# Performance work log

Hardware: AMD Instinct MI355X
Metric: run time of the kernel (lower is better)

Reference implementation:

```python
import jax, jax.numpy as jnp
import numpy as np


def setup_inputs() -> dict:
    key = jax.random.key(0)
    ks = jax.random.split(key, 8)
    Bsz, L, D, N, R = 2, 2048, 2048, 16, 128
    x = jax.random.normal(ks[0], (Bsz, L, D), jnp.float32)
    delta = jax.random.normal(ks[1], (Bsz, L, R), jnp.float32)
    B_in = jax.random.normal(ks[2], (Bsz, L, N), jnp.float32)
    C_in = jax.random.normal(ks[3], (Bsz, L, N), jnp.float32)
    # dt_proj params (scaled small so softplus(dt) stays in a sane range)
    W_dt = jax.random.normal(ks[4], (D, R), jnp.float32) * 0.02
    b_dt = jax.random.normal(ks[5], (D,), jnp.float32) * 0.02
    # A_log = log(uniform(0,1)) as in the torch init -> A = -exp(A_log) in (-1, 0)
    A_log = jnp.log(jax.random.uniform(ks[6], (D, N), jnp.float32, 1e-4, 1.0))
    D_param = jnp.ones((D,), jnp.float32)
    return {"x": x, "delta": delta, "B_in": B_in, "C_in": C_in,
            "W_dt": W_dt, "b_dt": b_dt, "A_log": A_log, "D_param": D_param}


def reference(x, delta, B_in, C_in, W_dt, b_dt, A_log, D_param):
    # dt = softplus(dt_proj(delta))  -> (B, L, D)
    dt = jax.nn.softplus(jnp.einsum('blr,dr->bld', delta, W_dt) + b_dt)
    A = -jnp.exp(A_log)                                  # (D, N)
    decay = jnp.exp(jnp.einsum('bld,dn->bldn', dt, A))   # exp(dt*A): (B, L, D, N)
    u = jnp.einsum('bld,bln->bldn', dt * x, B_in)        # dt*B*x input term
    # move length to leading axis for scan
    aT = jnp.moveaxis(decay, 1, 0)   # (L, B, D, N)
    uT = jnp.moveaxis(u, 1, 0)       # (L, B, D, N)
    cT = jnp.moveaxis(C_in, 1, 0)    # (L, B, N)

    h0 = jnp.zeros((x.shape[0], x.shape[2], A.shape[1]), x.dtype)  # (B, D, N)

    def step(h, inp):
        a, uu, c = inp
        h = a * h + uu                              # selective state update
        y = jnp.einsum('bdn,bn->bd', h, c)          # readout
        return h, y

    _, ys = jax.lax.scan(step, h0, (aT, uT, cT))    # ys: (L, B, D)
    return jnp.moveaxis(ys, 0, 1) + x * D_param
```

## Files before the change

### kernel.cpp

```cpp
#include <hip/hip_runtime.h>
#include <hip/hip_bf16.h>
#include <math.h>

namespace {

constexpr int BSZ = 2, LEN = 2048, DIM = 2048, NST = 16, RNK = 128;
constexpr int NC = 64, CHUNK = LEN / NC;
constexpr int KS = 3 * RNK;
constexpr float LOG2E = 1.4426950408889634f;
constexpr float LN2 = 0.6931471805599453f;

using bf16x8 = __attribute__((ext_vector_type(8))) short;
using f32x4  = __attribute__((ext_vector_type(4))) float;

__device__ __forceinline__ float fast_exp2(float x) {
#if __has_builtin(__builtin_amdgcn_exp2f)
  return __builtin_amdgcn_exp2f(x);
#else
  return exp2f(x);
#endif
}

__device__ __forceinline__ unsigned short bf16_rne(float x) {
  __hip_bfloat16 h = __float2bfloat16(x);
  return *(unsigned short*)&h;
}
__device__ __forceinline__ float bf16_tof(unsigned short u) {
  __hip_bfloat16 h = *(__hip_bfloat16*)&u;
  return __bfloat162float(h);
}

__global__ __launch_bounds__(256)
void split_bf16(const float* __restrict__ delta, const float* __restrict__ W,
                unsigned short* __restrict__ Ad, unsigned short* __restrict__ Bd) {
  int t = blockIdx.x * 256 + threadIdx.x;
  const int NA = BSZ * LEN * RNK;
  if (t < NA) {
    int row = t >> 7, k = t & (RNK - 1);
    float x = delta[t];
    unsigned short hi = bf16_rne(x);
    unsigned short lo = bf16_rne(x - bf16_tof(hi));
    unsigned short* p = Ad + (size_t)row * KS;
    p[k] = hi; p[RNK + k] = lo; p[2 * RNK + k] = hi;
  } else {
    t -= NA;
    int row = t >> 7, k = t & (RNK - 1);
    float x = W[t];
    unsigned short hi = bf16_rne(x);
    unsigned short lo = bf16_rne(x - bf16_tof(hi));
    unsigned short* p = Bd + (size_t)row * KS;
    p[k] = hi; p[RNK + k] = hi; p[2 * RNK + k] = lo;
  }
}

__global__ __launch_bounds__(256)
void dt_mfma(const unsigned short* __restrict__ Ad, const unsigned short* __restrict__ Bd,
             const float* __restrict__ bias, float* __restrict__ dtout) {
  const int lane = threadIdx.x & 63, wid = threadIdx.x >> 6;
  const int wm = wid >> 1, wn = wid & 1;
  const int bm = blockIdx.x & 31, bn = blockIdx.x >> 5;
  const int r = lane & 15, kg = lane >> 4;

  const unsigned short* arow = Ad + (size_t)(bm * 128 + wm * 64 + r) * KS + kg * 8;
  const unsigned short* brow = Bd + (size_t)(bn * 128 + wn * 64 + r) * KS + kg * 8;

  f32x4 acc[4][4] = {};
#pragma unroll
  for (int ks = 0; ks < KS / 32; ++ks) {
    bf16x8 af[4], bf[4];
#pragma unroll
    for (int m = 0; m < 4; ++m)
      af[m] = *(const bf16x8*)(arow + (size_t)m * 16 * KS + ks * 32);
#pragma unroll
    for (int n = 0; n < 4; ++n)
      bf[n] = *(const bf16x8*)(brow + (size_t)n * 16 * KS + ks * 32);
#pragma unroll
    for (int m = 0; m < 4; ++m)
#pragma unroll
      for (int n = 0; n < 4; ++n)
        acc[m][n] = __builtin_amdgcn_mfma_f32_16x16x32_bf16(af[m], bf[n], acc[m][n], 0, 0, 0);
  }

#pragma unroll
  for (int n = 0; n < 4; ++n) {
    const int col = bn * 128 + wn * 64 + n * 16 + r;
    const float bs = bias[col];
#pragma unroll
    for (int m = 0; m < 4; ++m) {
      const int row0 = bm * 128 + wm * 64 + m * 16 + kg * 4;
#pragma unroll
      for (int j = 0; j < 4; ++j) {
        float z = acc[m][n][j] + bs;
        float sp = fmaxf(z, 0.f) + LN2 * __log2f(1.0f + fast_exp2(-fabsf(z) * LOG2E));
        dtout[(size_t)(row0 + j) * DIM + col] = sp;
      }
    }
  }
}

__global__ __launch_bounds__(256)
void scan_pass1(const float* __restrict__ dtw, const float* __restrict__ x,
                const float* __restrict__ Bin, const float* __restrict__ Alog,
                float* __restrict__ Pout, float* __restrict__ Sout) {
  __shared__ float4 Bl[CHUNK * NST / 4];
  const int tid = threadIdx.x;
  const int bz = blockIdx.x;
  const int dt8 = bz & 7;
  const int c = (bz >> 3) & (NC - 1);
  const int b = bz >> 9;
  const int d = dt8 * 256 + tid;
  const int l0 = c * CHUNK;

  if (tid < CHUNK * NST / 4)
    Bl[tid] = ((const float4*)(Bin + ((size_t)b * LEN + l0) * NST))[tid];

  float A2[NST];
  {
    const float4* ap = (const float4*)(Alog + (size_t)d * NST);
#pragma unroll
    for (int q = 0; q < 4; ++q) {
      float4 v = ap[q];
      A2[q * 4 + 0] = -expf(v.x) * LOG2E;
      A2[q * 4 + 1] = -expf(v.y) * LOG2E;
      A2[q * 4 + 2] = -expf(v.z) * LOG2E;
      A2[q * 4 + 3] = -expf(v.w) * LOG2E;
    }
  }
  __syncthreads();

  float h[NST];
#pragma unroll
  for (int n = 0; n < NST; ++n) h[n] = 0.f;
  float sdt = 0.f;
  const float* dtp = dtw + ((size_t)b * LEN + l0) * DIM + d;
  const float* xp  = x   + ((size_t)b * LEN + l0) * DIM + d;

  float dtc = dtp[0], xc = xp[0];
#pragma unroll 4
  for (int i = 0; i < CHUNK; ++i) {
    float dtn = 0.f, xn = 0.f;
    if (i + 1 < CHUNK) { dtn = dtp[(size_t)(i + 1) * DIM]; xn = xp[(size_t)(i + 1) * DIM]; }
    float dtx = dtc * xc;
    sdt += dtc;
#pragma unroll
    for (int q = 0; q < 4; ++q) {
      float4 Bv = Bl[i * 4 + q];
      float e0 = fast_exp2(dtc * A2[q * 4 + 0]);
      float e1 = fast_exp2(dtc * A2[q * 4 + 1]);
      float e2 = fast_exp2(dtc * A2[q * 4 + 2]);
      float e3 = fast_exp2(dtc * A2[q * 4 + 3]);
      h[q * 4 + 0] = fmaf(e0, h[q * 4 + 0], dtx * Bv.x);
      h[q * 4 + 1] = fmaf(e1, h[q * 4 + 1], dtx * Bv.y);
      h[q * 4 + 2] = fmaf(e2, h[q * 4 + 2], dtx * Bv.z);
      h[q * 4 + 3] = fmaf(e3, h[q * 4 + 3], dtx * Bv.w);
    }
    dtc = dtn; xc = xn;
  }

  const size_t obase = ((size_t)(b * NC + c) * DIM + d) * NST;
#pragma unroll
  for (int q = 0; q < 4; ++q) {
    float4 pv;
    pv.x = fast_exp2(sdt * A2[q * 4 + 0]);
    pv.y = fast_exp2(sdt * A2[q * 4 + 1]);
    pv.z = fast_exp2(sdt * A2[q * 4 + 2]);
    pv.w = fast_exp2(sdt * A2[q * 4 + 3]);
    *(float4*)&Pout[obase + q * 4] = pv;
    float4 sv = {h[q * 4 + 0], h[q * 4 + 1], h[q * 4 + 2], h[q * 4 + 3]};
    *(float4*)&Sout[obase + q * 4] = sv;
  }
}

__global__ __launch_bounds__(256)
void chunk_combine(float* __restrict__ P, const float* __restrict__ S) {
  const int t = blockIdx.x * 256 + threadIdx.x;
  const int n = t & (NST - 1);
  const int d = (t >> 4) & (DIM - 1);
  const int b = t >> 15;
  float cur = 0.f;
#pragma unroll 8
  for (int c = 0; c < NC; ++c) {
    const size_t idx = ((size_t)(b * NC + c) * DIM + d) * NST + n;
    float p = P[idx];
    float s = S[idx];
    P[idx] = cur;
    cur = fmaf(p, cur, s);
  }
}

__global__ __launch_bounds__(256)
void scan_pass2(const float* __restrict__ dtw, const float* __restrict__ x,
                const float* __restrict__ Bin, const float* __restrict__ Cin,
                const float* __restrict__ Alog, const float* __restrict__ Dpar,
                const float* __restrict__ Hin, float* __restrict__ out) {
  __shared__ float4 Bl[CHUNK * NST / 4];
  __shared__ float4 Cl[CHUNK * NST / 4];
  const int tid = threadIdx.x;
  const int bz = blockIdx.x;
  const int dt8 = bz & 7;
  const int c = (bz >> 3) & (NC - 1);
  const int b = bz >> 9;
  const int d = dt8 * 256 + tid;
  const int l0 = c * CHUNK;

  if (tid < CHUNK * NST / 4)
    Bl[tid] = ((const float4*)(Bin + ((size_t)b * LEN + l0) * NST))[tid];
  else if (tid < CHUNK * NST / 2)
    Cl[tid - CHUNK * NST / 4] = ((const float4*)(Cin + ((size_t)b * LEN + l0) * NST))[tid - CHUNK * NST / 4];

  float A2[NST];
  {
    const float4* ap = (const float4*)(Alog + (size_t)d * NST);
#pragma unroll
    for (int q = 0; q < 4; ++q) {
      float4 v = ap[q];
      A2[q * 4 + 0] = -expf(v.x) * LOG2E;
      A2[q * 4 + 1] = -expf(v.y) * LOG2E;
      A2[q * 4 + 2] = -expf(v.z) * LOG2E;
      A2[q * 4 + 3] = -expf(v.w) * LOG2E;
    }
  }

  const size_t obase = ((size_t)(b * NC + c) * DIM + d) * NST;
  float h[NST];
#pragma unroll
  for (int q = 0; q < 4; ++q) {
    float4 hv = *(const float4*)&Hin[obase + q * 4];
    h[q * 4 + 0] = hv.x; h[q * 4 + 1] = hv.y; h[q * 4 + 2] = hv.z; h[q * 4 + 3] = hv.w;
  }
  const float dpar = Dpar[d];
  __syncthreads();

  const float* dtp = dtw + ((size_t)b * LEN + l0) * DIM + d;
  const float* xp  = x   + ((size_t)b * LEN + l0) * DIM + d;
  float* op        = out + ((size_t)b * LEN + l0) * DIM + d;

  float dtc = dtp[0], xc = xp[0];
#pragma unroll 4
  for (int i = 0; i < CHUNK; ++i) {
    float dtn = 0.f, xn = 0.f;
    if (i + 1 < CHUNK) { dtn = dtp[(size_t)(i + 1) * DIM]; xn = xp[(size_t)(i + 1) * DIM]; }
    float dtx = dtc * xc;
    float y0 = 0.f, y1 = 0.f, y2 = 0.f, y3 = 0.f;
#pragma unroll
    for (int q = 0; q < 4; ++q) {
      float4 Bv = Bl[i * 4 + q];
      float4 Cv = Cl[i * 4 + q];
      float e0 = fast_exp2(dtc * A2[q * 4 + 0]);
      float e1 = fast_exp2(dtc * A2[q * 4 + 1]);
      float e2 = fast_exp2(dtc * A2[q * 4 + 2]);
      float e3 = fast_exp2(dtc * A2[q * 4 + 3]);
      float hh0 = fmaf(e0, h[q * 4 + 0], dtx * Bv.x);
      float hh1 = fmaf(e1, h[q * 4 + 1], dtx * Bv.y);
      float hh2 = fmaf(e2, h[q * 4 + 2], dtx * Bv.z);
      float hh3 = fmaf(e3, h[q * 4 + 3], dtx * Bv.w);
      h[q * 4 + 0] = hh0; h[q * 4 + 1] = hh1; h[q * 4 + 2] = hh2; h[q * 4 + 3] = hh3;
      float yq = hh0 * Cv.x;
      yq = fmaf(hh1, Cv.y, yq);
      yq = fmaf(hh2, Cv.z, yq);
      yq = fmaf(hh3, Cv.w, yq);
      if (q == 0) y0 = yq; else if (q == 1) y1 = yq; else if (q == 2) y2 = yq; else y3 = yq;
    }
    op[(size_t)i * DIM] = fmaf(xc, dpar, (y0 + y1) + (y2 + y3));
    dtc = dtn; xc = xn;
  }
}

}

extern "C" void kernel_launch(void* const* d_in, const int* in_sizes, int n_in,
                              void* d_out, int out_size, void* d_ws, size_t ws_size,
                              hipStream_t stream) {
  const float* x     = (const float*)d_in[0];
  const float* delta = (const float*)d_in[1];
  const float* Bin   = (const float*)d_in[2];
  const float* Cin   = (const float*)d_in[3];
  const float* Wdt   = (const float*)d_in[4];
  const float* bdt   = (const float*)d_in[5];
  const float* Alog  = (const float*)d_in[6];
  const float* Dpar  = (const float*)d_in[7];
  float* out = (float*)d_out;

  char* ws = (char*)d_ws;
  size_t off = 0;
  float* dtw = (float*)(ws + off); off += (size_t)BSZ * LEN * DIM * 4;
  float* P   = (float*)(ws + off); off += (size_t)BSZ * NC * DIM * NST * 4;
  float* S   = (float*)(ws + off); off += (size_t)BSZ * NC * DIM * NST * 4;
  unsigned short* Ad = (unsigned short*)(ws + off); off += (size_t)BSZ * LEN * KS * 2;
  unsigned short* Bd = (unsigned short*)(ws + off); off += (size_t)DIM * KS * 2;

  split_bf16<<<(BSZ * LEN * RNK + DIM * RNK) / 256, 256, 0, stream>>>(delta, Wdt, Ad, Bd);
  dt_mfma<<<(BSZ * LEN / 128) * (DIM / 128), 256, 0, stream>>>(Ad, Bd, bdt, dtw);
  scan_pass1<<<BSZ * NC * (DIM / 256), 256, 0, stream>>>(dtw, x, Bin, Alog, P, S);
  chunk_combine<<<BSZ * DIM * NST / 256, 256, 0, stream>>>(P, S);
  scan_pass2<<<BSZ * NC * (DIM / 256), 256, 0, stream>>>(dtw, x, Bin, Cin, Alog, Dpar, P, out);
}
```

Measured before the change: 185.0 us.

## Fuse dt projection GEMM into both scan passes and drop P buffer

Removes the standalone dt GEMM kernel and its 32 MB dt workspace. Each scan block now recomputes its 32x256 dt tile with MFMA into shared memory, and both passes read dt from LDS instead of global memory. Pass 1 also writes only the per-chunk sum of dt instead of the full decay product P, and chunk_combine rebuilds the decay from Alog. The cost is running the GEMM twice (once per pass) and using 32 KB of extra LDS per block, which may lower occupancy.

```diff
diff --git a/kernel.cpp b/kernel.cpp
--- a/kernel.cpp
+++ b/kernel.cpp
@@ -53,66 +53,66 @@
   }
 }
 
-__global__ __launch_bounds__(256)
-void dt_mfma(const unsigned short* __restrict__ Ad, const unsigned short* __restrict__ Bd,
-             const float* __restrict__ bias, float* __restrict__ dtout) {
-  const int lane = threadIdx.x & 63, wid = threadIdx.x >> 6;
-  const int wm = wid >> 1, wn = wid & 1;
-  const int bm = blockIdx.x & 31, bn = blockIdx.x >> 5;
+__device__ __forceinline__ void compute_dt_tile(
+    const unsigned short* __restrict__ Ad, const unsigned short* __restrict__ Bd,
+    const float* __restrict__ bias, int b, int l0, int dgrp,
+    float (*dt_tile)[256]) {
+  const int lane = threadIdx.x & 63, w = threadIdx.x >> 6;
   const int r = lane & 15, kg = lane >> 4;
-
-  const unsigned short* arow = Ad + (size_t)(bm * 128 + wm * 64 + r) * KS + kg * 8;
-  const unsigned short* brow = Bd + (size_t)(bn * 128 + wn * 64 + r) * KS + kg * 8;
-
-  f32x4 acc[4][4] = {};
+  const unsigned short* arow = Ad + (size_t)(b * LEN + l0 + r) * KS + kg * 8;
+  const unsigned short* brow = Bd + (size_t)(dgrp * 256 + w * 64 + r) * KS + kg * 8;
+
+  f32x4 acc[2][4] = {};
 #pragma unroll
   for (int ks = 0; ks < KS / 32; ++ks) {
-    bf16x8 af[4], bf[4];
-#pragma unroll
-    for (int m = 0; m < 4; ++m)
-      af[m] = *(const bf16x8*)(arow + (size_t)m * 16 * KS + ks * 32);
+    bf16x8 af[2], bfr[4];
+    af[0] = *(const bf16x8*)(arow + ks * 32);
+    af[1] = *(const bf16x8*)(arow + (size_t)16 * KS + ks * 32);
 #pragma unroll
     for (int n = 0; n < 4; ++n)
-      bf[n] = *(const bf16x8*)(brow + (size_t)n * 16 * KS + ks * 32);
-#pragma unroll
-    for (int m = 0; m < 4; ++m)
+      bfr[n] = *(const bf16x8*)(brow + (size_t)n * 16 * KS + ks * 32);
+#pragma unroll
+    for (int m = 0; m < 2; ++m)
 #pragma unroll
       for (int n = 0; n < 4; ++n)
-        acc[m][n] = __builtin_amdgcn_mfma_f32_16x16x32_bf16(af[m], bf[n], acc[m][n], 0, 0, 0);
-  }
-
+        acc[m][n] = __builtin_amdgcn_mfma_f32_16x16x32_bf16(af[m], bfr[n], acc[m][n], 0, 0, 0);
+  }
 #pragma unroll
   for (int n = 0; n < 4; ++n) {
-    const int col = bn * 128 + wn * 64 + n * 16 + r;
-    const float bs = bias[col];
-#pragma unroll
-    for (int m = 0; m < 4; ++m) {
-      const int row0 = bm * 128 + wm * 64 + m * 16 + kg * 4;
+    const int dl = w * 64 + n * 16 + r;
+    const float bs = bias[dgrp * 256 + dl];
+#pragma unroll
+    for (int m = 0; m < 2; ++m) {
+      const int row0 = m * 16 + kg * 4;
 #pragma unroll
       for (int j = 0; j < 4; ++j) {
         float z = acc[m][n][j] + bs;
         float sp = fmaxf(z, 0.f) + LN2 * __log2f(1.0f + fast_exp2(-fabsf(z) * LOG2E));
-        dtout[(size_t)(row0 + j) * DIM + col] = sp;
+        dt_tile[row0 + j][dl] = sp;
       }
     }
   }
 }
 
 __global__ __launch_bounds__(256)
-void scan_pass1(const float* __restrict__ dtw, const float* __restrict__ x,
-                const float* __restrict__ Bin, const float* __restrict__ Alog,
-                float* __restrict__ Pout, float* __restrict__ Sout) {
+void scan1_fused(const unsigned short* __restrict__ Ad, const unsigned short* __restrict__ Bd,
+                 const float* __restrict__ bias, const float* __restrict__ x,
+                 const float* __restrict__ Bin, const float* __restrict__ Alog,
+                 float* __restrict__ Sout, float* __restrict__ sdtout) {
+  __shared__ float dt_tile[CHUNK][256];
   __shared__ float4 Bl[CHUNK * NST / 4];
   const int tid = threadIdx.x;
   const int bz = blockIdx.x;
-  const int dt8 = bz & 7;
+  const int dgrp = bz & 7;
   const int c = (bz >> 3) & (NC - 1);
   const int b = bz >> 9;
-  const int d = dt8 * 256 + tid;
+  const int d = dgrp * 256 + tid;
   const int l0 = c * CHUNK;
 
   if (tid < CHUNK * NST / 4)
     Bl[tid] = ((const float4*)(Bin + ((size_t)b * LEN + l0) * NST))[tid];
+
+  compute_dt_tile(Ad, Bd, bias, b, l0, dgrp, dt_tile);
 
   float A2[NST];
   {
@@ -132,81 +132,82 @@
 #pragma unroll
   for (int n = 0; n < NST; ++n) h[n] = 0.f;
   float sdt = 0.f;
-  const float* dtp = dtw + ((size_t)b * LEN + l0) * DIM + d;
-  const float* xp  = x   + ((size_t)b * LEN + l0) * DIM + d;
-
-  float dtc = dtp[0], xc = xp[0];
+  const float* xp = x + ((size_t)b * LEN + l0) * DIM + d;
+
+  float xc = xp[0];
 #pragma unroll 4
   for (int i = 0; i < CHUNK; ++i) {
-    float dtn = 0.f, xn = 0.f;
-    if (i + 1 < CHUNK) { dtn = dtp[(size_t)(i + 1) * DIM]; xn = xp[(size_t)(i + 1) * DIM]; }
-    float dtx = dtc * xc;
-    sdt += dtc;
+    float xn = 0.f;
+    if (i + 1 < CHUNK) xn = xp[(size_t)(i + 1) * DIM];
+    float dt = dt_tile[i][tid];
+    float dtx = dt * xc;
+    sdt += dt;
 #pragma unroll
     for (int q = 0; q < 4; ++q) {
       float4 Bv = Bl[i * 4 + q];
-      float e0 = fast_exp2(dtc * A2[q * 4 + 0]);
-      float e1 = fast_exp2(dtc * A2[q * 4 + 1]);
-      float e2 = fast_exp2(dtc * A2[q * 4 + 2]);
-      float e3 = fast_exp2(dtc * A2[q * 4 + 3]);
+      float e0 = fast_exp2(dt * A2[q * 4 + 0]);
+      float e1 = fast_exp2(dt * A2[q * 4 + 1]);
+      float e2 = fast_exp2(dt * A2[q * 4 + 2]);
+      float e3 = fast_exp2(dt * A2[q * 4 + 3]);
       h[q * 4 + 0] = fmaf(e0, h[q * 4 + 0], dtx * Bv.x);
       h[q * 4 + 1] = fmaf(e1, h[q * 4 + 1], dtx * Bv.y);
       h[q * 4 + 2] = fmaf(e2, h[q * 4 + 2], dtx * Bv.z);
       h[q * 4 + 3] = fmaf(e3, h[q * 4 + 3], dtx * Bv.w);
     }
-    dtc = dtn; xc = xn;
+    xc = xn;
   }
 
   const size_t obase = ((size_t)(b * NC + c) * DIM + d) * NST;
 #pragma unroll
   for (int q = 0; q < 4; ++q) {
-    float4 pv;
-    pv.x = fast_exp2(sdt * A2[q * 4 + 0]);
-    pv.y = fast_exp2(sdt * A2[q * 4 + 1]);
-    pv.z = fast_exp2(sdt * A2[q * 4 + 2]);
-    pv.w = fast_exp2(sdt * A2[q * 4 + 3]);
-    *(float4*)&Pout[obase + q * 4] = pv;
     float4 sv = {h[q * 4 + 0], h[q * 4 + 1], h[q * 4 + 2], h[q * 4 + 3]};
     *(float4*)&Sout[obase + q * 4] = sv;
   }
-}
-
-__global__ __launch_bounds__(256)
-void chunk_combine(float* __restrict__ P, const float* __restrict__ S) {
+  sdtout[(size_t)(b * NC + c) * DIM + d] = sdt;
+}
+
+__global__ __launch_bounds__(256)
+void chunk_combine(const float* __restrict__ sdt, float* __restrict__ S,
+                   const float* __restrict__ Alog) {
   const int t = blockIdx.x * 256 + threadIdx.x;
   const int n = t & (NST - 1);
   const int d = (t >> 4) & (DIM - 1);
   const int b = t >> 15;
+  const float a2 = -expf(Alog[(size_t)d * NST + n]) * LOG2E;
   float cur = 0.f;
 #pragma unroll 8
   for (int c = 0; c < NC; ++c) {
     const size_t idx = ((size_t)(b * NC + c) * DIM + d) * NST + n;
-    float p = P[idx];
     float s = S[idx];
-    P[idx] = cur;
-    cur = fmaf(p, cur, s);
-  }
-}
-
-__global__ __launch_bounds__(256)
-void scan_pass2(const float* __restrict__ dtw, const float* __restrict__ x,
-                const float* __restrict__ Bin, const float* __restrict__ Cin,
-                const float* __restrict__ Alog, const float* __restrict__ Dpar,
-                const float* __restrict__ Hin, float* __restrict__ out) {
+    float sd = sdt[(size_t)(b * NC + c) * DIM + d];
+    S[idx] = cur;
+    cur = fmaf(fast_exp2(sd * a2), cur, s);
+  }
+}
+
+__global__ __launch_bounds__(256)
+void scan2_fused(const unsigned short* __restrict__ Ad, const unsigned short* __restrict__ Bd,
+                 const float* __restrict__ bias, const float* __restrict__ x,
+                 const float* __restrict__ Bin, const float* __restrict__ Cin,
+                 const float* __restrict__ Alog, const float* __restrict__ Dpar,
+                 const float* __restrict__ Hin, float* __restrict__ out) {
+  __shared__ float dt_tile[CHUNK][256];
   __shared__ float4 Bl[CHUNK * NST / 4];
   __shared__ float4 Cl[CHUNK * NST / 4];
   const int tid = threadIdx.x;
   const int bz = blockIdx.x;
-  const int dt8 = bz & 7;
+  const int dgrp = bz & 7;
   const int c = (bz >> 3) & (NC - 1);
   const int b = bz >> 9;
-  const int d = dt8 * 256 + tid;
+  const int d = dgrp * 256 + tid;
   const int l0 = c * CHUNK;
 
   if (tid < CHUNK * NST / 4)
     Bl[tid] = ((const float4*)(Bin + ((size_t)b * LEN + l0) * NST))[tid];
   else if (tid < CHUNK * NST / 2)
     Cl[tid - CHUNK * NST / 4] = ((const float4*)(Cin + ((size_t)b * LEN + l0) * NST))[tid - CHUNK * NST / 4];
+
+  compute_dt_tile(Ad, Bd, bias, b, l0, dgrp, dt_tile);
 
   float A2[NST];
   {
@@ -231,25 +232,25 @@
   const float dpar = Dpar[d];
   __syncthreads();
 
-  const float* dtp = dtw + ((size_t)b * LEN + l0) * DIM + d;
-  const float* xp  = x   + ((size_t)b * LEN + l0) * DIM + d;
-  float* op        = out + ((size_t)b * LEN + l0) * DIM + d;
-
-  float dtc = dtp[0], xc = xp[0];
+  const float* xp = x + ((size_t)b * LEN + l0) * DIM + d;
+  float* op       = out + ((size_t)b * LEN + l0) * DIM + d;
+
+  float xc = xp[0];
 #pragma unroll 4
   for (int i = 0; i < CHUNK; ++i) {
-    float dtn = 0.f, xn = 0.f;
-    if (i + 1 < CHUNK) { dtn = dtp[(size_t)(i + 1) * DIM]; xn = xp[(size_t)(i + 1) * DIM]; }
-    float dtx = dtc * xc;
+    float xn = 0.f;
+    if (i + 1 < CHUNK) xn = xp[(size_t)(i + 1) * DIM];
+    float dt = dt_tile[i][tid];
+    float dtx = dt * xc;
     float y0 = 0.f, y1 = 0.f, y2 = 0.f, y3 = 0.f;
 #pragma unroll
     for (int q = 0; q < 4; ++q) {
       float4 Bv = Bl[i * 4 + q];
       float4 Cv = Cl[i * 4 + q];
-      float e0 = fast_exp2(dtc * A2[q * 4 + 0]);
-      float e1 = fast_exp2(dtc * A2[q * 4 + 1]);
-      float e2 = fast_exp2(dtc * A2[q * 4 + 2]);
-      float e3 = fast_exp2(dtc * A2[q * 4 + 3]);
+      float e0 = fast_exp2(dt * A2[q * 4 + 0]);
+      float e1 = fast_exp2(dt * A2[q * 4 + 1]);
+      float e2 = fast_exp2(dt * A2[q * 4 + 2]);
+      float e3 = fast_exp2(dt * A2[q * 4 + 3]);
       float hh0 = fmaf(e0, h[q * 4 + 0], dtx * Bv.x);
       float hh1 = fmaf(e1, h[q * 4 + 1], dtx * Bv.y);
       float hh2 = fmaf(e2, h[q * 4 + 2], dtx * Bv.z);
@@ -262,7 +263,7 @@
       if (q == 0) y0 = yq; else if (q == 1) y1 = yq; else if (q == 2) y2 = yq; else y3 = yq;
     }
     op[(size_t)i * DIM] = fmaf(xc, dpar, (y0 + y1) + (y2 + y3));
-    dtc = dtn; xc = xn;
+    xc = xn;
   }
 }
 
@@ -283,15 +284,13 @@
 
   char* ws = (char*)d_ws;
   size_t off = 0;
-  float* dtw = (float*)(ws + off); off += (size_t)BSZ * LEN * DIM * 4;
-  float* P   = (float*)(ws + off); off += (size_t)BSZ * NC * DIM * NST * 4;
   float* S   = (float*)(ws + off); off += (size_t)BSZ * NC * DIM * NST * 4;
+  float* sdt = (float*)(ws + off); off += (size_t)BSZ * NC * DIM * 4;
   unsigned short* Ad = (unsigned short*)(ws + off); off += (size_t)BSZ * LEN * KS * 2;
   unsigned short* Bd = (unsigned short*)(ws + off); off += (size_t)DIM * KS * 2;
 
   split_bf16<<<(BSZ * LEN * RNK + DIM * RNK) / 256, 256, 0, stream>>>(delta, Wdt, Ad, Bd);
-  dt_mfma<<<(BSZ * LEN / 128) * (DIM / 128), 256, 0, stream>>>(Ad, Bd, bdt, dtw);
-  scan_pass1<<<BSZ * NC * (DIM / 256), 256, 0, stream>>>(dtw, x, Bin, Alog, P, S);
-  chunk_combine<<<BSZ * DIM * NST / 256, 256, 0, stream>>>(P, S);
-  scan_pass2<<<BSZ * NC * (DIM / 256), 256, 0, stream>>>(dtw, x, Bin, Cin, Alog, Dpar, P, out);
-}
+  scan1_fused<<<BSZ * NC * (DIM / 256), 256, 0, stream>>>(Ad, Bd, bdt, x, Bin, Alog, S, sdt);
+  chunk_combine<<<BSZ * DIM * NST / 256, 256, 0, stream>>>(sdt, S, Alog);
+  scan2_fused<<<BSZ * NC * (DIM / 256), 256, 0, stream>>>(Ad, Bd, bdt, x, Bin, Cin, Alog, Dpar, S, out);
+}
```

After: 211.2 us. 14.1% more time.

## Split scan state dimension across threads and stage chunk inputs in LDS

Applied to the files above, without the earlier changes.

Both scan passes now assign 8 threads per channel, each owning 2 of the 16 state entries, so each block covers 32 channels and there are 8x more blocks. dt, x, B and C for the chunk are staged in shared memory, and the readout is reduced with width-8 shuffles. The P buffer is replaced by a per-chunk dt sum, and chunk_combine recomputes the decay with exp2 while prefetching 8 chunks ahead. The aim is more parallelism and less per-thread serial exp work, in exchange for shuffle overhead, more redundant dt/x loads and 7/8 idle lanes on the output stores.

```diff
diff --git a/kernel.cpp b/kernel.cpp
--- a/kernel.cpp
+++ b/kernel.cpp
@@ -99,170 +99,149 @@
 }
 
 __global__ __launch_bounds__(256)
-void scan_pass1(const float* __restrict__ dtw, const float* __restrict__ x,
-                const float* __restrict__ Bin, const float* __restrict__ Alog,
-                float* __restrict__ Pout, float* __restrict__ Sout) {
-  __shared__ float4 Bl[CHUNK * NST / 4];
+void scan1_ns(const float* __restrict__ dtw, const float* __restrict__ x,
+              const float* __restrict__ Bin, const float* __restrict__ Alog,
+              float* __restrict__ Sout, float* __restrict__ sdtout) {
+  __shared__ float dt_l[CHUNK][32];
+  __shared__ float x_l[CHUNK][32];
+  __shared__ float B_l[CHUNK][NST];
   const int tid = threadIdx.x;
   const int bz = blockIdx.x;
-  const int dt8 = bz & 7;
-  const int c = (bz >> 3) & (NC - 1);
-  const int b = bz >> 9;
-  const int d = dt8 * 256 + tid;
+  const int dgrp = bz & 63;
+  const int c = (bz >> 6) & (NC - 1);
+  const int b = bz >> 12;
   const int l0 = c * CHUNK;
-
-  if (tid < CHUNK * NST / 4)
-    Bl[tid] = ((const float4*)(Bin + ((size_t)b * LEN + l0) * NST))[tid];
-
-  float A2[NST];
-  {
-    const float4* ap = (const float4*)(Alog + (size_t)d * NST);
-#pragma unroll
-    for (int q = 0; q < 4; ++q) {
-      float4 v = ap[q];
-      A2[q * 4 + 0] = -expf(v.x) * LOG2E;
-      A2[q * 4 + 1] = -expf(v.y) * LOG2E;
-      A2[q * 4 + 2] = -expf(v.z) * LOG2E;
-      A2[q * 4 + 3] = -expf(v.w) * LOG2E;
-    }
-  }
+  const int nt = tid & 7, dl = tid >> 3;
+  const int d = dgrp * 32 + dl;
+  const int n0 = nt * 2;
+
+  const float* dtp = dtw + ((size_t)b * LEN + l0) * DIM + dgrp * 32;
+  const float* xp  = x   + ((size_t)b * LEN + l0) * DIM + dgrp * 32;
+#pragma unroll
+  for (int j = 0; j < 4; ++j) {
+    int idx = tid + j * 256, row = idx >> 5, col = idx & 31;
+    dt_l[row][col] = dtp[(size_t)row * DIM + col];
+    x_l[row][col]  = xp[(size_t)row * DIM + col];
+  }
+#pragma unroll
+  for (int j = 0; j < 2; ++j) {
+    int idx = tid + j * 256, row = idx >> 4, nn = idx & 15;
+    B_l[row][nn] = Bin[((size_t)b * LEN + l0 + row) * NST + nn];
+  }
+  float2 al = *(const float2*)&Alog[(size_t)d * NST + n0];
+  const float a20 = -expf(al.x) * LOG2E;
+  const float a21 = -expf(al.y) * LOG2E;
   __syncthreads();
 
-  float h[NST];
-#pragma unroll
-  for (int n = 0; n < NST; ++n) h[n] = 0.f;
-  float sdt = 0.f;
-  const float* dtp = dtw + ((size_t)b * LEN + l0) * DIM + d;
-  const float* xp  = x   + ((size_t)b * LEN + l0) * DIM + d;
-
-  float dtc = dtp[0], xc = xp[0];
-#pragma unroll 4
+  float h0 = 0.f, h1 = 0.f, sdt = 0.f;
+#pragma unroll
   for (int i = 0; i < CHUNK; ++i) {
-    float dtn = 0.f, xn = 0.f;
-    if (i + 1 < CHUNK) { dtn = dtp[(size_t)(i + 1) * DIM]; xn = xp[(size_t)(i + 1) * DIM]; }
-    float dtx = dtc * xc;
-    sdt += dtc;
-#pragma unroll
-    for (int q = 0; q < 4; ++q) {
-      float4 Bv = Bl[i * 4 + q];
-      float e0 = fast_exp2(dtc * A2[q * 4 + 0]);
-      float e1 = fast_exp2(dtc * A2[q * 4 + 1]);
-      float e2 = fast_exp2(dtc * A2[q * 4 + 2]);
-      float e3 = fast_exp2(dtc * A2[q * 4 + 3]);
-      h[q * 4 + 0] = fmaf(e0, h[q * 4 + 0], dtx * Bv.x);
-      h[q * 4 + 1] = fmaf(e1, h[q * 4 + 1], dtx * Bv.y);
-      h[q * 4 + 2] = fmaf(e2, h[q * 4 + 2], dtx * Bv.z);
-      h[q * 4 + 3] = fmaf(e3, h[q * 4 + 3], dtx * Bv.w);
-    }
-    dtc = dtn; xc = xn;
-  }
-
-  const size_t obase = ((size_t)(b * NC + c) * DIM + d) * NST;
-#pragma unroll
-  for (int q = 0; q < 4; ++q) {
-    float4 pv;
-    pv.x = fast_exp2(sdt * A2[q * 4 + 0]);
-    pv.y = fast_exp2(sdt * A2[q * 4 + 1]);
-    pv.z = fast_exp2(sdt * A2[q * 4 + 2]);
-    pv.w = fast_exp2(sdt * A2[q * 4 + 3]);
-    *(float4*)&Pout[obase + q * 4] = pv;
-    float4 sv = {h[q * 4 + 0], h[q * 4 + 1], h[q * 4 + 2], h[q * 4 + 3]};
-    *(float4*)&Sout[obase + q * 4] = sv;
-  }
-}
-
-__global__ __launch_bounds__(256)
-void chunk_combine(float* __restrict__ P, const float* __restrict__ S) {
+    float dt = dt_l[i][dl];
+    float dtx = dt * x_l[i][dl];
+    sdt += dt;
+    float e0 = fast_exp2(dt * a20);
+    float e1 = fast_exp2(dt * a21);
+    h0 = fmaf(e0, h0, dtx * B_l[i][n0]);
+    h1 = fmaf(e1, h1, dtx * B_l[i][n0 + 1]);
+  }
+  const size_t ob = ((size_t)(b * NC + c) * DIM + d) * NST + n0;
+  float2 hv; hv.x = h0; hv.y = h1;
+  *(float2*)&Sout[ob] = hv;
+  if (nt == 0) sdtout[(size_t)(b * NC + c) * DIM + d] = sdt;
+}
+
+__global__ __launch_bounds__(256)
+void chunk_combine(const float* __restrict__ sdt, float* __restrict__ S,
+                   const float* __restrict__ Alog) {
   const int t = blockIdx.x * 256 + threadIdx.x;
   const int n = t & (NST - 1);
   const int d = (t >> 4) & (DIM - 1);
   const int b = t >> 15;
+  const float a2 = -expf(Alog[(size_t)d * NST + n]) * LOG2E;
+
+  float pfS[8], pfD[8];
+#pragma unroll
+  for (int c = 0; c < 8; ++c) {
+    const size_t idx = ((size_t)(b * NC + c) * DIM + d) * NST + n;
+    pfS[c] = S[idx];
+    pfD[c] = sdt[(size_t)(b * NC + c) * DIM + d];
+  }
   float cur = 0.f;
-#pragma unroll 8
+#pragma unroll
   for (int c = 0; c < NC; ++c) {
     const size_t idx = ((size_t)(b * NC + c) * DIM + d) * NST + n;
-    float p = P[idx];
-    float s = S[idx];
-    P[idx] = cur;
-    cur = fmaf(p, cur, s);
-  }
-}
-
-__global__ __launch_bounds__(256)
-void scan_pass2(const float* __restrict__ dtw, const float* __restrict__ x,
-                const float* __restrict__ Bin, const float* __restrict__ Cin,
-                const float* __restrict__ Alog, const float* __restrict__ Dpar,
-                const float* __restrict__ Hin, float* __restrict__ out) {
-  __shared__ float4 Bl[CHUNK * NST / 4];
-  __shared__ float4 Cl[CHUNK * NST / 4];
+    float s = pfS[c & 7];
+    float sd = pfD[c & 7];
+    S[idx] = cur;
+    if (c + 8 < NC) {
+      const size_t idx8 = ((size_t)(b * NC + c + 8) * DIM + d) * NST + n;
+      pfS[c & 7] = S[idx8];
+      pfD[c & 7] = sdt[(size_t)(b * NC + c + 8) * DIM + d];
+    }
+    cur = fmaf(fast_exp2(sd * a2), cur, s);
+  }
+}
+
+__global__ __launch_bounds__(256)
+void scan2_ns(const float* __restrict__ dtw, const float* __restrict__ x,
+              const float* __restrict__ Bin, const float* __restrict__ Cin,
+              const float* __restrict__ Alog, const float* __restrict__ Dpar,
+              const float* __restrict__ Hin, float* __restrict__ out) {
+  __shared__ float dt_l[CHUNK][32];
+  __shared__ float x_l[CHUNK][32];
+  __shared__ float B_l[CHUNK][NST];
+  __shared__ float C_l[CHUNK][NST];
   const int tid = threadIdx.x;
   const int bz = blockIdx.x;
-  const int dt8 = bz & 7;
-  const int c = (bz >> 3) & (NC - 1);
-  const int b = bz >> 9;
-  const int d = dt8 * 256 + tid;
+  const int dgrp = bz & 63;
+  const int c = (bz >> 6) & (NC - 1);
+  const int b = bz >> 12;
   const int l0 = c * CHUNK;
-
-  if (tid < CHUNK * NST / 4)
-    Bl[tid] = ((const float4*)(Bin + ((size_t)b * LEN + l0) * NST))[tid];
-  else if (tid < CHUNK * NST / 2)
-    Cl[tid - CHUNK * NST / 4] = ((const float4*)(Cin + ((size_t)b * LEN + l0) * NST))[tid - CHUNK * NST / 4];
-
-  float A2[NST];
-  {
-    const float4* ap = (const float4*)(Alog + (size_t)d * NST);
-#pragma unroll
-    for (int q = 0; q < 4; ++q) {
-      float4 v = ap[q];
-      A2[q * 4 + 0] = -expf(v.x) * LOG2E;
-      A2[q * 4 + 1] = -expf(v.y) * LOG2E;
-      A2[q * 4 + 2] = -expf(v.z) * LOG2E;
-      A2[q * 4 + 3] = -expf(v.w) * LOG2E;
-    }
-  }
-
-  const size_t obase = ((size_t)(b * NC + c) * DIM + d) * NST;
-  float h[NST];
-#pragma unroll
-  for (int q = 0; q < 4; ++q) {
-    float4 hv = *(const float4*)&Hin[obase + q * 4];
-    h[q * 4 + 0] = hv.x; h[q * 4 + 1] = hv.y; h[q * 4 + 2] = hv.z; h[q * 4 + 3] = hv.w;
-  }
+  const int nt = tid & 7, dl = tid >> 3;
+  const int d = dgrp * 32 + dl;
+  const int n0 = nt * 2;
+
+  const float* dtp = dtw + ((size_t)b * LEN + l0) * DIM + dgrp * 32;
+  const float* xp  = x   + ((size_t)b * LEN + l0) * DIM + dgrp * 32;
+#pragma unroll
+  for (int j = 0; j < 4; ++j) {
+    int idx = tid + j * 256, row = idx >> 5, col = idx & 31;
+    dt_l[row][col] = dtp[(size_t)row * DIM + col];
+    x_l[row][col]  = xp[(size_t)row * DIM + col];
+  }
+#pragma unroll
+  for (int j = 0; j < 2; ++j) {
+    int idx = tid + j * 256, row = idx >> 4, nn = idx & 15;
+    B_l[row][nn] = Bin[((size_t)b * LEN + l0 + row) * NST + nn];
+    C_l[row][nn] = Cin[((size_t)b * LEN + l0 + row) * NST + nn];
+  }
+  float2 al = *(const float2*)&Alog[(size_t)d * NST + n0];
+  const float a20 = -expf(al.x) * LOG2E;
+  const float a21 = -expf(al.y) * LOG2E;
   const float dpar = Dpar[d];
+
+  const size_t ob = ((size_t)(b * NC + c) * DIM + d) * NST + n0;
+  float2 hv = *(const float2*)&Hin[ob];
+  float h0 = hv.x, h1 = hv.y;
   __syncthreads();
 
-  const float* dtp = dtw + ((size_t)b * LEN + l0) * DIM + d;
-  const float* xp  = x   + ((size_t)b * LEN + l0) * DIM + d;
-  float* op        = out + ((size_t)b * LEN + l0) * DIM + d;
-
-  float dtc = dtp[0], xc = xp[0];
-#pragma unroll 4
+  float* op = out + ((size_t)b * LEN + l0) * DIM + d;
+
+#pragma unroll
   for (int i = 0; i < CHUNK; ++i) {
-    float dtn = 0.f, xn = 0.f;
-    if (i + 1 < CHUNK) { dtn = dtp[(size_t)(i + 1) * DIM]; xn = xp[(size_t)(i + 1) * DIM]; }
-    float dtx = dtc * xc;
-    float y0 = 0.f, y1 = 0.f, y2 = 0.f, y3 = 0.f;
-#pragma unroll
-    for (int q = 0; q < 4; ++q) {
-      float4 Bv = Bl[i * 4 + q];
-      float4 Cv = Cl[i * 4 + q];
-      float e0 = fast_exp2(dtc * A2[q * 4 + 0]);
-      float e1 = fast_exp2(dtc * A2[q * 4 + 1]);
-      float e2 = fast_exp2(dtc * A2[q * 4 + 2]);
-      float e3 = fast_exp2(dtc * A2[q * 4 + 3]);
-      float hh0 = fmaf(e0, h[q * 4 + 0], dtx * Bv.x);
-      float hh1 = fmaf(e1, h[q * 4 + 1], dtx * Bv.y);
-      float hh2 = fmaf(e2, h[q * 4 + 2], dtx * Bv.z);
-      float hh3 = fmaf(e3, h[q * 4 + 3], dtx * Bv.w);
-      h[q * 4 + 0] = hh0; h[q * 4 + 1] = hh1; h[q * 4 + 2] = hh2; h[q * 4 + 3] = hh3;
-      float yq = hh0 * Cv.x;
-      yq = fmaf(hh1, Cv.y, yq);
-      yq = fmaf(hh2, Cv.z, yq);
-      yq = fmaf(hh3, Cv.w, yq);
-      if (q == 0) y0 = yq; else if (q == 1) y1 = yq; else if (q == 2) y2 = yq; else y3 = yq;
-    }
-    op[(size_t)i * DIM] = fmaf(xc, dpar, (y0 + y1) + (y2 + y3));
-    dtc = dtn; xc = xn;
+    float dt = dt_l[i][dl];
+    float xv = x_l[i][dl];
+    float dtx = dt * xv;
+    float e0 = fast_exp2(dt * a20);
+    float e1 = fast_exp2(dt * a21);
+    h0 = fmaf(e0, h0, dtx * B_l[i][n0]);
+    h1 = fmaf(e1, h1, dtx * B_l[i][n0 + 1]);
+    float yp = h0 * C_l[i][n0];
+    yp = fmaf(h1, C_l[i][n0 + 1], yp);
+    yp += __shfl_xor(yp, 1, 8);
+    yp += __shfl_xor(yp, 2, 8);
+    yp += __shfl_xor(yp, 4, 8);
+    if (nt == 0) op[(size_t)i * DIM] = fmaf(xv, dpar, yp);
   }
 }
 
@@ -284,14 +263,14 @@
   char* ws = (char*)d_ws;
   size_t off = 0;
   float* dtw = (float*)(ws + off); off += (size_t)BSZ * LEN * DIM * 4;
-  float* P   = (float*)(ws + off); off += (size_t)BSZ * NC * DIM * NST * 4;
   float* S   = (float*)(ws + off); off += (size_t)BSZ * NC * DIM * NST * 4;
+  float* sdt = (float*)(ws + off); off += (size_t)BSZ * NC * DIM * 4;
   unsigned short* Ad = (unsigned short*)(ws + off); off += (size_t)BSZ * LEN * KS * 2;
   unsigned short* Bd = (unsigned short*)(ws + off); off += (size_t)DIM * KS * 2;
 
   split_bf16<<<(BSZ * LEN * RNK + DIM * RNK) / 256, 256, 0, stream>>>(delta, Wdt, Ad, Bd);
   dt_mfma<<<(BSZ * LEN / 128) * (DIM / 128), 256, 0, stream>>>(Ad, Bd, bdt, dtw);
-  scan_pass1<<<BSZ * NC * (DIM / 256), 256, 0, stream>>>(dtw, x, Bin, Alog, P, S);
-  chunk_combine<<<BSZ * DIM * NST / 256, 256, 0, stream>>>(P, S);
-  scan_pass2<<<BSZ * NC * (DIM / 256), 256, 0, stream>>>(dtw, x, Bin, Cin, Alog, Dpar, P, out);
-}
+  scan1_ns<<<BSZ * NC * (DIM / 32), 256, 0, stream>>>(dtw, x, Bin, Alog, S, sdt);
+  chunk_combine<<<BSZ * DIM * NST / 256, 256, 0, stream>>>(sdt, S, Alog);
+  scan2_ns<<<BSZ * NC * (DIM / 32), 256, 0, stream>>>(dtw, x, Bin, Cin, Alog, Dpar, S, out);
+}
```

After: 200.1 us. +8.1%, slower.
